# Performance work log

Hardware: AMD Instinct MI355X
Metric: run time of the kernel (lower is better)

The kernel has to match this reference:

```python
import jax, jax.numpy as jnp
import numpy as np

H = 32      # query heads
KV = 8      # kv heads
D = 128     # head_dim
HID = 4096
S = 4       # num sequences
L = 1024    # tokens per sequence
N = S * L   # total tokens
EPS = 1e-6
THETA = 10000.0
GROUPS = H // KV


def setup_inputs() -> dict:
    key = jax.random.key(0)
    ks = jax.random.split(key, 12)
    def w(k, shape, std):
        return jax.random.normal(k, shape, dtype=jnp.float32) * std
    return {
        "hidden": w(ks[0], (N, HID), 1.0),
        "mu_prev": w(ks[1], (N, HID), 1.0),
        "positions": jnp.tile(jnp.arange(L, dtype=jnp.int32), S),
        "Wq": w(ks[2], (H * D, HID), HID ** -0.5),
        "Wk": w(ks[3], (KV * D, HID), HID ** -0.5),
        "Wv": w(ks[4], (KV * D, HID), HID ** -0.5),
        "Wo": w(ks[5], (HID, H * D), (H * D) ** -0.5),
        "Wmq": w(ks[6], (H * D, HID), 0.01),
        "Wmk": w(ks[7], (KV * D, HID), 0.01),
        "Wmv": w(ks[8], (KV * D, HID), 0.01),
        "q_norm_w": jnp.ones((D,), jnp.float32),
        "k_norm_w": jnp.ones((D,), jnp.float32),
    }


def _rmsnorm(x, w):
    var = jnp.mean(jnp.square(x), axis=-1, keepdims=True)
    return x * jax.lax.rsqrt(var + EPS) * w


def _rope_cos_sin(positions):
    inv_freq = 1.0 / (THETA ** (jnp.arange(0, D, 2, dtype=jnp.float32) / D))  # [D/2]
    freqs = positions.astype(jnp.float32)[:, None] * inv_freq[None, :]        # [N, D/2]
    emb = jnp.concatenate([freqs, freqs], axis=-1)                            # [N, D]
    return jnp.cos(emb), jnp.sin(emb)


def _rotate_half(x):
    x1, x2 = jnp.split(x, 2, axis=-1)
    return jnp.concatenate([-x2, x1], axis=-1)


def _apply_rotary(x, cos, sin):
    # x: [N, h, D]; cos/sin: [N, D]
    return x * cos[:, None, :] + _rotate_half(x) * sin[:, None, :]


def reference(hidden, mu_prev, positions, Wq, Wk, Wv, Wo, Wmq, Wmk, Wmv, q_norm_w, k_norm_w):
    # QKV projections + mu-bias fusion
    q = hidden @ Wq.T + mu_prev @ Wmq.T     # [N, H*D]
    k = hidden @ Wk.T + mu_prev @ Wmk.T     # [N, KV*D]
    v = hidden @ Wv.T + mu_prev @ Wmv.T     # [N, KV*D]
    q = q.reshape(N, H, D)
    k = k.reshape(N, KV, D)
    v = v.reshape(N, KV, D)
    # QK RMSNorm
    q = _rmsnorm(q, q_norm_w)
    k = _rmsnorm(k, k_norm_w)
    # RoPE
    cos, sin = _rope_cos_sin(positions)
    q = _apply_rotary(q, cos, sin)
    k = _apply_rotary(k, cos, sin)
    # GQA: expand kv heads to match q heads
    k = jnp.repeat(k, GROUPS, axis=1)       # [N, H, D]
    v = jnp.repeat(v, GROUPS, axis=1)
    # Varlen causal attention: equal-length seqs -> batched [S, L, H, D]
    qs = q.reshape(S, L, H, D)
    ks = k.reshape(S, L, H, D)
    vs = v.reshape(S, L, H, D)
    scale = 1.0 / np.sqrt(D)
    scores = jnp.einsum("slhd,smhd->shlm", qs, ks) * scale   # [S, H, L, L]
    causal = jnp.tril(jnp.ones((L, L), dtype=bool))
    scores = jnp.where(causal, scores, jnp.finfo(scores.dtype).min)
    probs = jax.nn.softmax(scores, axis=-1)
    out = jnp.einsum("shlm,smhd->slhd", probs, vs)           # [S, L, H, D]
    out = out.reshape(N, H * D)
    return out @ Wo.T                                         # [N, HID]
```

## Files before the change

### kernel.cpp

```cpp
#include <hip/hip_runtime.h>
#include <hip/hip_bf16.h>
#include <stdint.h>

#define DEV static __device__ __forceinline__

typedef __bf16 bf16_t;
typedef __bf16 bf16x8 __attribute__((ext_vector_type(8)));
typedef __bf16 bf16x4 __attribute__((ext_vector_type(4)));
typedef float  f32x4  __attribute__((ext_vector_type(4)));


DEV void gload_lds16(const void* g, void* l) {
  __builtin_amdgcn_global_load_lds(
      (__attribute__((address_space(1))) void*)(uintptr_t)(g),
      (__attribute__((address_space(3))) void*)(uintptr_t)(l),
      16, 0, 0);
}

#define BARRIER() asm volatile("s_barrier" ::: "memory")
#define MFMA16(a, b, c) __builtin_amdgcn_mfma_f32_16x16x32_bf16((a), (b), (c), 0, 0, 0)

DEV void pack_pair_chunk(const float* __restrict__ A, const float* __restrict__ B,
                         bf16_t* __restrict__ dst, size_t i) {
  size_t r = i >> 10, c = i & 1023;
  float4 va = ((const float4*)A)[i];
  float4 vb = ((const float4*)B)[i];
  bf16x4 oa = {(bf16_t)va.x, (bf16_t)va.y, (bf16_t)va.z, (bf16_t)va.w};
  bf16x4 ob = {(bf16_t)vb.x, (bf16_t)vb.y, (bf16_t)vb.z, (bf16_t)vb.w};
  ((bf16x4*)dst)[r * 2048 + c] = oa;
  ((bf16x4*)dst)[r * 2048 + 1024 + c] = ob;
}

__global__ void k_pack_all(const float* __restrict__ hidden, const float* __restrict__ mu,
                           const float* __restrict__ Wq, const float* __restrict__ Wmq,
                           const float* __restrict__ Wk, const float* __restrict__ Wmk,
                           const float* __restrict__ Wv, const float* __restrict__ Wmv,
                           const float* __restrict__ Wo,
                           bf16_t* __restrict__ Xb, bf16_t* __restrict__ Wqkv,
                           bf16_t* __restrict__ Wob) {
  const size_t t0 = 4194304, t1 = 8388608, t2 = 9437184, t3 = 10485760, t4 = 14680064;
  size_t stride = (size_t)gridDim.x * blockDim.x;
  for (size_t i = (size_t)blockIdx.x * blockDim.x + threadIdx.x; i < t4; i += stride) {
    if (i < t0) {
      pack_pair_chunk(hidden, mu, Xb, i);
    } else if (i < t1) {
      pack_pair_chunk(Wq, Wmq, Wqkv, i - t0);
    } else if (i < t2) {
      pack_pair_chunk(Wk, Wmk, Wqkv + (size_t)4096 * 8192, i - t1);
    } else if (i < t3) {
      pack_pair_chunk(Wv, Wmv, Wqkv + (size_t)5120 * 8192, i - t2);
    } else {
      size_t j = i - t3;
      float4 v = ((const float4*)Wo)[j];
      bf16x4 o = {(bf16_t)v.x, (bf16_t)v.y, (bf16_t)v.z, (bf16_t)v.w};
      ((bf16x4*)Wob)[j] = o;
    }
  }
}

template<typename CT, int NSPLIT>
__global__ __launch_bounds__(512, 2) void k_gemm256(
    const bf16_t* __restrict__ A, const bf16_t* __restrict__ B,
    CT* __restrict__ C, int M, int N, int Kfull) {
  __shared__ __align__(16) char lds[131072];
  const int tid = threadIdx.x, lane = tid & 63, wid = tid >> 6;
  const int l15 = lane & 15, lhi = lane >> 4;
  const int wr = wid >> 2, wc = wid & 3;
  const int bid = blockIdx.x, nwg = gridDim.x;
  const int cpx = nwg >> 3;
  const int swz = (bid & 7) * cpx + (bid >> 3);
  const int nbm = M >> 8;
  const int tiles = nbm * (N >> 8);
  const int ks = (NSPLIT > 1) ? (swz / tiles) : 0;
  const int t  = (NSPLIT > 1) ? (swz % tiles) : swz;
  const int bm = t % nbm, bn = t / nbm;
  const int Kloop = Kfull / NSPLIT;
  const int nkt = Kloop >> 6;

  const size_t rowK = (size_t)Kfull * 2;
  const size_t kbase = (size_t)ks * Kloop * 2;
  const int off0 = wid * 1024 + lane * 16, off1 = off0 + 8192;
  const int r0 = off0 >> 7, r1 = off1 >> 7;
  const int c0 = ((off0 >> 4) & 7) ^ (r0 & 7);
  const int c1 = ((off1 >> 4) & 7) ^ (r1 & 7);
  const char* sA0 = (const char*)A + ((size_t)bm * 256 + r0) * rowK + kbase + c0 * 16;
  const char* sA1 = (const char*)A + ((size_t)bm * 256 + r1) * rowK + kbase + c1 * 16;
  const char* sB0 = (const char*)B + ((size_t)bn * 256 + r0) * rowK + kbase + c0 * 16;
  const char* sB1 = (const char*)B + ((size_t)bn * 256 + r1) * rowK + kbase + c1 * 16;
  const size_t hst = (size_t)128 * rowK;

  enum { A0S = 0, A1S = 16384, A2S = 32768, A3S = 49152,
         B0S = 65536, B1S = 81920, B2S = 98304, B3S = 114688 };

#define STG(slot, pa, pb, off) do { \
    gload_lds16((pa) + (off), lds + (slot) + wid * 1024); \
    gload_lds16((pb) + (off), lds + (slot) + 8192 + wid * 1024); } while (0)

  const bf16_t* Ae = (const bf16_t*)(lds + A0S + wr * 16384);
  const bf16_t* Be = (const bf16_t*)(lds + B0S + (wc >> 1) * 16384);
  const bf16_t* Ao = (const bf16_t*)(lds + A2S + wr * 16384);
  const bf16_t* Bo = (const bf16_t*)(lds + B2S + (wc >> 1) * 16384);
  const int bro = (wc & 1) * 64;

  f32x4 acc[8][4] = {};
  bf16x8 a[4][2], b[4][2];
  const int xr = l15 & 7;
  const int ck0 = (lhi ^ xr) * 8;
  const int ck1 = ((4 + lhi) ^ xr) * 8;

#define RD_A(base, rb) do { _Pragma("unroll") \
    for (int mi = 0; mi < 4; ++mi) { \
      const int ro = ((rb) + mi * 16 + l15) * 64; \
      a[mi][0] = *(const bf16x8*)((base) + ro + ck0); \
      a[mi][1] = *(const bf16x8*)((base) + ro + ck1); } } while (0)
#define RD_B(base) do { _Pragma("unroll") \
    for (int n = 0; n < 4; ++n) { \
      const int ro = (bro + n * 16 + l15) * 64; \
      b[n][0] = *(const bf16x8*)((base) + ro + ck0); \
      b[n][1] = *(const bf16x8*)((base) + ro + ck1); } } while (0)
#define MM(qm, qn) do { _Pragma("unroll") \
    for (int mi = 0; mi < 4; ++mi) { _Pragma("unroll") \
      for (int ni = 0; ni < 2; ++ni) { \
        f32x4 t_ = acc[(qm) * 4 + mi][(qn) * 2 + ni]; \
        t_ = MFMA16(a[mi][0], b[(qn) * 2 + ni][0], t_); \
        t_ = MFMA16(a[mi][1], b[(qn) * 2 + ni][1], t_); \
        acc[(qm) * 4 + mi][(qn) * 2 + ni] = t_; } } } while (0)
#define PRIO_MM(qm, qn) do { __builtin_amdgcn_s_setprio(1); MM(qm, qn); \
    __builtin_amdgcn_s_setprio(0); } while (0)

  STG(B0S, sB0, sB1, 0);
  STG(B1S, sB0, sB1, hst);
  STG(A0S, sA0, sA1, 0);
  STG(A1S, sA0, sA1, hst);
  STG(B2S, sB0, sB1, 128);
  STG(B3S, sB0, sB1, 128 + hst);
  STG(A2S, sA0, sA1, 128);
  asm volatile("s_waitcnt vmcnt(6)" ::: "memory");
  BARRIER();

  size_t g = 0;
  for (int ktp = 0; ktp < nkt / 2 - 1; ++ktp) {
    RD_A(Ae, 0); RD_B(Be);
    STG(A3S, sA0, sA1, g + 128 + hst);
    asm volatile("s_waitcnt lgkmcnt(8)" ::: "memory");
    BARRIER();
    PRIO_MM(0, 0);
    BARRIER();
    STG(B0S, sB0, sB1, g + 256);
    BARRIER();
    PRIO_MM(0, 1);
    BARRIER();
    RD_A(Ae, 64);
    STG(B1S, sB0, sB1, g + 256 + hst);
    BARRIER();
    PRIO_MM(1, 0);
    BARRIER();
    STG(A0S, sA0, sA1, g + 256);
    BARRIER();
    PRIO_MM(1, 1);
    asm volatile("s_waitcnt vmcnt(6)" ::: "memory");
    BARRIER();
    RD_A(Ao, 0); RD_B(Bo);
    STG(A1S, sA0, sA1, g + 256 + hst);
    asm volatile("s_waitcnt lgkmcnt(8)" ::: "memory");
    BARRIER();
    PRIO_MM(0, 0);
    BARRIER();
    STG(B2S, sB0, sB1, g + 384);
    BARRIER();
    PRIO_MM(0, 1);
    BARRIER();
    RD_A(Ao, 64);
    STG(B3S, sB0, sB1, g + 384 + hst);
    BARRIER();
    PRIO_MM(1, 0);
    BARRIER();
    STG(A2S, sA0, sA1, g + 384);
    BARRIER();
    PRIO_MM(1, 1);
    asm volatile("s_waitcnt vmcnt(6)" ::: "memory");
    BARRIER();
    g += 256;
  }
  RD_A(Ae, 0); RD_B(Be);
  STG(A3S, sA0, sA1, g + 128 + hst);
  BARRIER();
  PRIO_MM(0, 0);
  PRIO_MM(0, 1);
  RD_A(Ae, 64);
  PRIO_MM(1, 0);
  PRIO_MM(1, 1);
  asm volatile("s_waitcnt vmcnt(0)" ::: "memory");
  BARRIER();
  RD_A(Ao, 0); RD_B(Bo);
  PRIO_MM(0, 0);
  PRIO_MM(0, 1);
  RD_A(Ao, 64);
  PRIO_MM(1, 0);
  PRIO_MM(1, 1);

  CT* Cp = C + (size_t)ks * M * N;
#pragma unroll
  for (int m = 0; m < 8; ++m) {
    const int row0 = bm * 256 + wr * 128 + m * 16 + 4 * lhi;
#pragma unroll
    for (int n = 0; n < 4; ++n) {
      const int col = bn * 256 + wc * 64 + n * 16 + l15;
#pragma unroll
      for (int i = 0; i < 4; ++i)
        Cp[(size_t)(row0 + i) * N + col] = (CT)acc[m][n][i];
    }
  }
#undef STG
#undef RD_A
#undef RD_B
#undef MM
#undef PRIO_MM
}

__global__ __launch_bounds__(256) void k_norm_rope(
    const bf16_t* __restrict__ qkvA, const bf16_t* __restrict__ qkvB,
    const int* __restrict__ pos,
    const float* __restrict__ qw, const float* __restrict__ kw,
    bf16_t* __restrict__ Q, bf16_t* __restrict__ Kk, bf16_t* __restrict__ V) {
  const int w = blockIdx.x * 4 + (threadIdx.x >> 6);
  const int lane = threadIdx.x & 63;
  const int n = w / 48, slot = w % 48;
  const bf16_t* rowA = qkvA + (size_t)n * 6144;
  const bf16_t* rowB = qkvB + (size_t)n * 6144;
  if (slot >= 40) {
    const int h2 = slot - 40;
    const int c = 5120 + h2 * 128 + lane;
    float x0 = (float)rowA[c] + (float)rowB[c];
    float x1 = (float)rowA[c + 64] + (float)rowB[c + 64];
    bf16_t* dst = V + ((size_t)n * 8 + h2) * 128;
    dst[lane] = (bf16_t)x0;
    dst[lane + 64] = (bf16_t)x1;
    return;
  }
  const bool isq = slot < 32;
  const int h = isq ? slot : slot - 32;
  const int coff = (isq ? h * 128 : 4096 + h * 128) + lane;
  float x0 = (float)rowA[coff] + (float)rowB[coff];
  float x1 = (float)rowA[coff + 64] + (float)rowB[coff + 64];
  float ss = x0 * x0 + x1 * x1;
#pragma unroll
  for (int m = 32; m; m >>= 1) ss += __shfl_xor(ss, m, 64);
  const float inv = rsqrtf(ss * (1.0f / 128.0f) + 1e-6f);
  const float* wgt = isq ? qw : kw;
  float y0 = x0 * inv * wgt[lane];
  float y1 = x1 * inv * wgt[lane + 64];
  const float ang = (float)pos[n] * expf((float)lane * -0.14391156608f);
  float sn, cs;
  sincosf(ang, &sn, &cs);
  float o0 = y0 * cs - y1 * sn;
  float o1 = y1 * cs + y0 * sn;
  bf16_t* dst = isq ? (Q + ((size_t)n * 32 + h) * 128) : (Kk + ((size_t)n * 8 + h) * 128);
  dst[lane] = (bf16_t)o0;
  dst[lane + 64] = (bf16_t)o1;
}

__global__ __launch_bounds__(256, 2) void k_attn(
    const bf16_t* __restrict__ Q, const bf16_t* __restrict__ Kk,
    const bf16_t* __restrict__ V, bf16_t* __restrict__ O) {
  __shared__ __align__(16) bf16_t Ks[64 * 128];
  __shared__ __align__(16) bf16_t Vt[128 * 72];
  __shared__ __align__(16) bf16_t Ps[4][32 * 72];
  const int b = blockIdx.x;
  const int qb = b & 7, h = (b >> 3) & 31, s = b >> 8;
  const int kvh = h >> 2;
  const int tid = threadIdx.x, lane = tid & 63, wid = tid >> 6;
  const int l15 = lane & 15, lhi = lane >> 4;

  bf16x8 qf[2][4];
  {
    const int qrow = qb * 128 + wid * 32;
#pragma unroll
    for (int mt = 0; mt < 2; mt++) {
      const size_t base = ((size_t)(s * 1024 + qrow + mt * 16 + l15) * 32 + h) * 128;
#pragma unroll
      for (int kc = 0; kc < 4; kc++)
        qf[mt][kc] = *(const bf16x8*)(Q + base + kc * 32 + 8 * lhi);
    }
  }
  f32x4 of[2][8] = {};
  float mx[2][4], li[2][4];
#pragma unroll
  for (int mt = 0; mt < 2; mt++)
#pragma unroll
    for (int i = 0; i < 4; i++) { mx[mt][i] = -1e30f; li[mt][i] = 0.f; }

  const int ktiles = (qb + 1) * 2;
  const int vr_base = tid >> 4;
  const int vd0 = (tid & 15) * 8;

  for (int kt = 0; kt < ktiles; kt++) {
    const int kv0 = kt * 64;
#pragma unroll
    for (int c = 0; c < 4; c++) {
      const int wb = wid * 4096 + c * 1024;
      const int o = wb + lane * 16;
      const int krow = o >> 8;
      const int ci = (o >> 4) & 15;
      const int cs = ci ^ (krow & 7);
      const char* src =
          (const char*)(Kk + ((size_t)(s * 1024 + kv0 + krow) * 8 + kvh) * 128) + cs * 16;
      gload_lds16(src, (char*)Ks + wb);
    }
#pragma unroll
    for (int c = 0; c < 4; c++) {
      const int r = c * 16 + vr_base;
      bf16x8 v = *(const bf16x8*)(V + ((size_t)(s * 1024 + kv0 + r) * 8 + kvh) * 128 + vd0);
#pragma unroll
      for (int j = 0; j < 8; j++) {
        const int d = vd0 + j;
        const int cc = (r >> 3) ^ ((d >> 3) & 7);
        Vt[d * 72 + cc * 8 + (r & 7)] = v[j];
      }
    }
    __syncthreads();

    f32x4 sf[2][4] = {};
#pragma unroll
    for (int kc = 0; kc < 4; kc++) {
      bf16x8 kf[4];
#pragma unroll
      for (int n = 0; n < 4; n++) {
        const int krow = n * 16 + l15;
        const int ci = (kc * 4 + lhi) ^ (krow & 7);
        kf[n] = *(const bf16x8*)(Ks + krow * 128 + ci * 8);
      }
#pragma unroll
      for (int mt = 0; mt < 2; mt++)
#pragma unroll
        for (int n = 0; n < 4; n++)
          sf[mt][n] = MFMA16(qf[mt][kc], kf[n], sf[mt][n]);
    }

    const bool masked = (kt >= 2 * qb);
    const float scale = 0.08838834764831845f;
    float pv[2][4][4];
#pragma unroll
    for (int mt = 0; mt < 2; mt++) {
#pragma unroll
      for (int i = 0; i < 4; i++) {
        float rm = -1e30f;
#pragma unroll
        for (int n = 0; n < 4; n++) {
          float sv = sf[mt][n][i] * scale;
          if (masked) {
            const int kvg = kv0 + n * 16 + l15;
            const int qg = qb * 128 + wid * 32 + mt * 16 + 4 * lhi + i;
            if (kvg > qg) sv = -1e30f;
          }
          pv[mt][n][i] = sv;
          rm = fmaxf(rm, sv);
        }
#pragma unroll
        for (int mm = 1; mm < 16; mm <<= 1) rm = fmaxf(rm, __shfl_xor(rm, mm, 64));
        const float nm = fmaxf(mx[mt][i], rm);
        float ts = 0.f;
#pragma unroll
        for (int n = 0; n < 4; n++) {
          float e = __expf(pv[mt][n][i] - nm);
          pv[mt][n][i] = e;
          ts += e;
        }
#pragma unroll
        for (int mm = 1; mm < 16; mm <<= 1) ts += __shfl_xor(ts, mm, 64);
        const float al = __expf(mx[mt][i] - nm);
        li[mt][i] = li[mt][i] * al + ts;
        mx[mt][i] = nm;
#pragma unroll
        for (int n = 0; n < 8; n++) of[mt][n][i] *= al;
      }
    }

    bf16_t* myP = &Ps[wid][0];
#pragma unroll
    for (int mt = 0; mt < 2; mt++)
#pragma unroll
      for (int n = 0; n < 4; n++)
#pragma unroll
        for (int i = 0; i < 4; i++)
          myP[(mt * 16 + 4 * lhi + i) * 72 + n * 16 + l15] = (bf16_t)pv[mt][n][i];

#pragma unroll
    for (int kc = 0; kc < 2; kc++) {
      bf16x8 pf[2];
#pragma unroll
      for (int mt = 0; mt < 2; mt++)
        pf[mt] = *(const bf16x8*)(myP + (mt * 16 + l15) * 72 + kc * 32 + 8 * lhi);
#pragma unroll
      for (int n = 0; n < 8; n++) {
        const int d = n * 16 + l15;
        const int cc = (kc * 4 + lhi) ^ ((d >> 3) & 7);
        bf16x8 vf = *(const bf16x8*)(Vt + d * 72 + cc * 8);
#pragma unroll
        for (int mt = 0; mt < 2; mt++)
          of[mt][n] = MFMA16(pf[mt], vf, of[mt][n]);
      }
    }
    __syncthreads();
  }

#pragma unroll
  for (int mt = 0; mt < 2; mt++) {
#pragma unroll
    for (int i = 0; i < 4; i++) {
      const float invl = 1.0f / li[mt][i];
      const int tokrow = qb * 128 + wid * 32 + mt * 16 + 4 * lhi + i;
      bf16_t* dst = O + (size_t)(s * 1024 + tokrow) * 4096 + h * 128;
#pragma unroll
      for (int n = 0; n < 8; n++)
        dst[n * 16 + l15] = (bf16_t)(of[mt][n][i] * invl);
    }
  }
}

extern "C" void kernel_launch(void* const* d_in, const int* in_sizes, int n_in,
                              void* d_out, int out_size, void* d_ws, size_t ws_size,
                              hipStream_t stream) {
  const float* hidden = (const float*)d_in[0];
  const float* mu     = (const float*)d_in[1];
  const int*   pos    = (const int*)d_in[2];
  const float* Wq  = (const float*)d_in[3];
  const float* Wk  = (const float*)d_in[4];
  const float* Wv  = (const float*)d_in[5];
  const float* Wo  = (const float*)d_in[6];
  const float* Wmq = (const float*)d_in[7];
  const float* Wmk = (const float*)d_in[8];
  const float* Wmv = (const float*)d_in[9];
  const float* qw  = (const float*)d_in[10];
  const float* kw  = (const float*)d_in[11];
  float* out = (float*)d_out;
  char* ws = (char*)d_ws;

  if (ws_size < 301989888u) return;

  bf16_t* Wqkv = (bf16_t*)(ws);
  bf16_t* Wob  = (bf16_t*)(ws + 100663296);
  bf16_t* Xb   = (bf16_t*)(ws + 134217728);
  bf16_t* Qb   = (bf16_t*)(ws + 134217728);
  bf16_t* Kb   = (bf16_t*)(ws + 167772160);
  bf16_t* Vb   = (bf16_t*)(ws + 176160768);
  bf16_t* qkvA = (bf16_t*)(ws + 201326592);
  bf16_t* qkvB = (bf16_t*)(ws + 251658240);
  bf16_t* Ob   = (bf16_t*)(ws + 201326592);

  k_pack_all<<<2048, 256, 0, stream>>>(hidden, mu, Wq, Wmq, Wk, Wmk, Wv, Wmv, Wo,
                                       Xb, Wqkv, Wob);
  k_gemm256<bf16_t, 2><<<768, 512, 0, stream>>>(Xb, Wqkv, qkvA, 4096, 6144, 8192);
  k_norm_rope<<<49152, 256, 0, stream>>>(qkvA, qkvB, pos, qw, kw, Qb, Kb, Vb);
  k_attn<<<1024, 256, 0, stream>>>(Qb, Kb, Vb, Ob);
  k_gemm256<float, 1><<<256, 512, 0, stream>>>(Ob, Wob, out, 4096, 4096, 4096);
}
```

Before: 783.4 us.

## Pre-transpose V globally, double-buffer K tiles, and reorder attention blocks heavy-first

Adds a separate kernel that writes V transposed to a workspace buffer, so attention reads V fragments straight from global memory instead of scattering them into LDS each tile. K tiles are now double-buffered in LDS with async global-to-LDS loads for the next tile issued before the current tile's compute, and a barrier only runs between iterations. The block index mapping is changed so the largest causal query blocks are scheduled first and heads that share a KV head sit near each other. The cost is an extra kernel launch plus V traffic, and V reads in the inner loop now come from global or L2 with strided rows, which could add latency.

```diff
diff --git a/kernel.cpp b/kernel.cpp
--- a/kernel.cpp
+++ b/kernel.cpp
@@ -260,14 +260,42 @@
   dst[lane + 64] = (bf16_t)o1;
 }
 
+__global__ __launch_bounds__(256) void k_vt(const bf16_t* __restrict__ V,
+                                            bf16_t* __restrict__ Vt) {
+  __shared__ bf16_t T[64][136];
+  const int blk = blockIdx.x;
+  const int tt = blk & 15, kvh = (blk >> 4) & 7, s = blk >> 7;
+  const int tok0 = tt * 64;
+  const int tid = threadIdx.x;
+#pragma unroll
+  for (int k = 0; k < 4; ++k) {
+    const int item = tid + k * 256;
+    const int tok = item >> 4, d0 = (item & 15) * 8;
+    bf16x8 v = *(const bf16x8*)(V + ((size_t)(s * 1024 + tok0 + tok) * 8 + kvh) * 128 + d0);
+    *(bf16x8*)(&T[tok][d0]) = v;
+  }
+  __syncthreads();
+#pragma unroll
+  for (int k = 0; k < 4; ++k) {
+    const int item = tid + k * 256;
+    const int d = item & 127, oct = item >> 7;
+    bf16x8 o;
+#pragma unroll
+    for (int j = 0; j < 8; ++j) o[j] = T[oct * 8 + j][d];
+    *(bf16x8*)(Vt + ((size_t)((s * 8 + kvh) * 128 + d)) * 1024 + tok0 + oct * 8) = o;
+  }
+}
+
 __global__ __launch_bounds__(256, 2) void k_attn(
     const bf16_t* __restrict__ Q, const bf16_t* __restrict__ Kk,
-    const bf16_t* __restrict__ V, bf16_t* __restrict__ O) {
-  __shared__ __align__(16) bf16_t Ks[64 * 128];
-  __shared__ __align__(16) bf16_t Vt[128 * 72];
+    const bf16_t* __restrict__ Vt, bf16_t* __restrict__ O) {
+  __shared__ __align__(16) bf16_t Ks[2][64 * 128];
   __shared__ __align__(16) bf16_t Ps[4][32 * 72];
   const int b = blockIdx.x;
-  const int qb = b & 7, h = (b >> 3) & 31, s = b >> 8;
+  const int x = b & 7, y = b >> 3;
+  const int h = x * 4 + ((y >> 3) & 3);
+  const int qb = 7 - (y & 7);
+  const int s = y >> 5;
   const int kvh = h >> 2;
   const int tid = threadIdx.x, lane = tid & 63, wid = tid >> 6;
   const int l15 = lane & 15, lhi = lane >> 4;
@@ -283,6 +311,8 @@
         qf[mt][kc] = *(const bf16x8*)(Q + base + kc * 32 + 8 * lhi);
     }
   }
+  const bf16_t* Vtb = Vt + (size_t)((s * 8 + kvh) * 128) * 1024;
+
   f32x4 of[2][8] = {};
   float mx[2][4], li[2][4];
 #pragma unroll
@@ -291,34 +321,26 @@
     for (int i = 0; i < 4; i++) { mx[mt][i] = -1e30f; li[mt][i] = 0.f; }
 
   const int ktiles = (qb + 1) * 2;
-  const int vr_base = tid >> 4;
-  const int vd0 = (tid & 15) * 8;
+
+  const int so = wid * 4096;
+#define STAGE_K(kt_, buf_) do { _Pragma("unroll") \
+    for (int c = 0; c < 4; ++c) { \
+      const int o = so + c * 1024 + lane * 16; \
+      const int krow = o >> 8; \
+      const int cs = ((o >> 4) & 15) ^ (krow & 7); \
+      const char* src = (const char*)(Kk + \
+          ((size_t)(s * 1024 + (kt_) * 64 + krow) * 8 + kvh) * 128) + cs * 16; \
+      gload_lds16(src, (char*)&Ks[buf_][0] + so + c * 1024); \
+    } } while (0)
+
+  STAGE_K(0, 0);
+  asm volatile("s_waitcnt vmcnt(0)" ::: "memory");
+  BARRIER();
 
   for (int kt = 0; kt < ktiles; kt++) {
     const int kv0 = kt * 64;
-#pragma unroll
-    for (int c = 0; c < 4; c++) {
-      const int wb = wid * 4096 + c * 1024;
-      const int o = wb + lane * 16;
-      const int krow = o >> 8;
-      const int ci = (o >> 4) & 15;
-      const int cs = ci ^ (krow & 7);
-      const char* src =
-          (const char*)(Kk + ((size_t)(s * 1024 + kv0 + krow) * 8 + kvh) * 128) + cs * 16;
-      gload_lds16(src, (char*)Ks + wb);
-    }
-#pragma unroll
-    for (int c = 0; c < 4; c++) {
-      const int r = c * 16 + vr_base;
-      bf16x8 v = *(const bf16x8*)(V + ((size_t)(s * 1024 + kv0 + r) * 8 + kvh) * 128 + vd0);
-#pragma unroll
-      for (int j = 0; j < 8; j++) {
-        const int d = vd0 + j;
-        const int cc = (r >> 3) ^ ((d >> 3) & 7);
-        Vt[d * 72 + cc * 8 + (r & 7)] = v[j];
-      }
-    }
-    __syncthreads();
+    const int buf = kt & 1;
+    if (kt + 1 < ktiles) STAGE_K(kt + 1, buf ^ 1);
 
     f32x4 sf[2][4] = {};
 #pragma unroll
@@ -328,7 +350,7 @@
       for (int n = 0; n < 4; n++) {
         const int krow = n * 16 + l15;
         const int ci = (kc * 4 + lhi) ^ (krow & 7);
-        kf[n] = *(const bf16x8*)(Ks + krow * 128 + ci * 8);
+        kf[n] = *(const bf16x8*)(&Ks[buf][0] + krow * 128 + ci * 8);
       }
 #pragma unroll
       for (int mt = 0; mt < 2; mt++)
@@ -394,15 +416,19 @@
 #pragma unroll
       for (int n = 0; n < 8; n++) {
         const int d = n * 16 + l15;
-        const int cc = (kc * 4 + lhi) ^ ((d >> 3) & 7);
-        bf16x8 vf = *(const bf16x8*)(Vt + d * 72 + cc * 8);
+        bf16x8 vf = *(const bf16x8*)(Vtb + (size_t)d * 1024 + kv0 + kc * 32 + 8 * lhi);
 #pragma unroll
         for (int mt = 0; mt < 2; mt++)
           of[mt][n] = MFMA16(pf[mt], vf, of[mt][n]);
       }
     }
-    __syncthreads();
-  }
+
+    if (kt + 1 < ktiles) {
+      asm volatile("s_waitcnt vmcnt(0)" ::: "memory");
+      BARRIER();
+    }
+  }
+#undef STAGE_K
 
 #pragma unroll
   for (int mt = 0; mt < 2; mt++) {
@@ -444,6 +470,7 @@
   bf16_t* Qb   = (bf16_t*)(ws + 134217728);
   bf16_t* Kb   = (bf16_t*)(ws + 167772160);
   bf16_t* Vb   = (bf16_t*)(ws + 176160768);
+  bf16_t* VtG  = (bf16_t*)(ws + 184549376);
   bf16_t* qkvA = (bf16_t*)(ws + 201326592);
   bf16_t* qkvB = (bf16_t*)(ws + 251658240);
   bf16_t* Ob   = (bf16_t*)(ws + 201326592);
@@ -452,6 +479,7 @@
                                        Xb, Wqkv, Wob);
   k_gemm256<bf16_t, 2><<<768, 512, 0, stream>>>(Xb, Wqkv, qkvA, 4096, 6144, 8192);
   k_norm_rope<<<49152, 256, 0, stream>>>(qkvA, qkvB, pos, qw, kw, Qb, Kb, Vb);
-  k_attn<<<1024, 256, 0, stream>>>(Qb, Kb, Vb, Ob);
+  k_vt<<<512, 256, 0, stream>>>(Vb, VtG);
+  k_attn<<<1024, 256, 0, stream>>>(Qb, Kb, VtG, Ob);
   k_gemm256<float, 1><<<256, 512, 0, stream>>>(Ob, Wob, out, 4096, 4096, 4096);
 }
```

Result: no change. 768.5 us (-1.9%).
